# Optimization experiments

Hardware: AMD Instinct MI355X
Metric: run time of the kernel (lower is better)

## Reference

```python
import jax, jax.numpy as jnp
import numpy as np

INV_TEMP = 10.0
_LOG_2PI = float(np.log(2.0 * np.pi))


def log_vmf_norm_const(kappa, dim):
    """log C_dim(kappa) = (dim/2-1)*log(kappa) - (dim/2)*log(2*pi) - log I_{dim/2-1}(kappa),
    with log I_v(kappa) via the uniform asymptotic expansion (as used in mkirchhof/url)."""
    v = dim / 2.0 - 1.0
    s = jnp.sqrt(v * v + kappa * kappa)
    log_iv = s + v * jnp.log(kappa / (v + s)) - 0.5 * _LOG_2PI - 0.25 * jnp.log(v * v + kappa * kappa)
    return v * jnp.log(kappa) - (dim / 2.0) * _LOG_2PI - log_iv


def _normalize(x, eps=1e-12):
    # matches torch F.normalize: x / max(||x||, eps)
    n = jnp.linalg.norm(x, axis=-1, keepdims=True)
    return x / jnp.maximum(n, eps)


def setup_inputs() -> dict:
    key = jax.random.key(0)
    kf, ku, ky, kw, kp = jax.random.split(key, 5)
    B, C, D = 2048, 16384, 128
    features = jax.random.normal(kf, (B, D), jnp.float32)
    unc = jax.random.uniform(ku, (B,), jnp.float32, minval=0.05, maxval=1.0)
    y = jax.random.randint(ky, (B,), 0, C)
    classifier_weight = jax.random.normal(kw, (C, D), jnp.float32)
    pred = jax.random.normal(kp, (B, C), jnp.float32)  # unused by the loss, kept for signature fidelity
    return {"pred": pred, "unc": unc, "y": y, "features": features,
            "classifier_weight": classifier_weight}


def reference(pred, unc, y, features, classifier_weight):
    dim = features.shape[-1]
    class_mu = _normalize(classifier_weight)                                  # [C, D]
    class_kappa = jnp.maximum(jnp.linalg.norm(classifier_weight, axis=-1), 1.0) * INV_TEMP  # [C]
    batch_mu = _normalize(features)                                           # [B, D]
    batch_kappa = 1.0 / unc                                                   # [B]

    # ||k1*mu1 + k2*mu2|| with unit mu's  ==  sqrt(k1^2 + k2^2 + 2*k1*k2*<mu1,mu2>)
    # (avoids the torch code's [B, C, D] broadcast; same math)
    dots = jnp.einsum('bd,cd->bc', batch_mu, class_mu)                        # [B, C]
    k1 = batch_kappa[:, None]                                                 # [B, 1]
    k2 = class_kappa[None, :]                                                 # [1, C]
    kappa3 = jnp.sqrt(jnp.maximum(k1 * k1 + k2 * k2 + 2.0 * k1 * k2 * dots, 1e-12))  # [B, C]

    sim = (log_vmf_norm_const(k1, dim) + log_vmf_norm_const(k2, dim)
           - log_vmf_norm_const(kappa3, dim))                                 # [B, C]

    gathered = jnp.take_along_axis(sim, y[:, None], axis=1)[:, 0]             # [B]
    lse = jax.nn.logsumexp(sim, axis=1)                                       # [B]
    return jnp.mean(-gathered + lse)
```

## Files before the change

kernel.cpp:

```cpp
#include <hip/hip_runtime.h>
#include <hip/hip_bf16.h>


typedef __bf16 bf16;
typedef __attribute__((ext_vector_type(8))) __bf16 bf16x8;
typedef __attribute__((ext_vector_type(4))) float f32x4;
typedef __attribute__((ext_vector_type(2))) float f32x2;

#define LOG2E 1.44269504088896340736f
#define LN2   0.69314718055994530942f
#define VNU   63.0f
#define VSQ   3969.0f

#if __has_builtin(__builtin_amdgcn_exp2f)
#define EXP2F(x) __builtin_amdgcn_exp2f(x)
#else
#define EXP2F(x) exp2f(x)
#endif
#if __has_builtin(__builtin_amdgcn_sqrtf)
#define SQRTF(x) __builtin_amdgcn_sqrtf(x)
#else
#define SQRTF(x) sqrtf(x)
#endif
#if __has_builtin(__builtin_amdgcn_logf)
#define LOG2F(x) __builtin_amdgcn_logf(x)
#else
#define LOG2F(x) __log2f(x)
#endif

#define QC0  289.4379f
#define QC1  -48.9193f
#define QC2  -2.9400f
#define QC3  0.51653f
#define QC4  -0.11373f

__global__ __launch_bounds__(256) void vmf_prep(
    const float* __restrict__ W, const float* __restrict__ feat,
    const float* __restrict__ unc,
    bf16* __restrict__ swW, bf16* __restrict__ swF,
    float4* __restrict__ cst, float* __restrict__ k1, int C, int B)
{
  const int lane = threadIdx.x & 63;
  const int idx  = blockIdx.x * 4 + (threadIdx.x >> 6);
  const bool is_class = idx < C;
  const int b = idx - C;
  const float* src;
  bf16* dstbase;
  int r;
  if (is_class) { src = W + (size_t)idx * 128;  dstbase = swW;  r = idx; }
  else {
    if (b >= B) return;
    src = feat + (size_t)b * 128;  dstbase = swF;  r = b;
  }
  float2 xv = reinterpret_cast<const float2*>(src)[lane];
  float ssq = fmaf(xv.x, xv.x, xv.y * xv.y);
  #pragma unroll
  for (int off = 32; off; off >>= 1) ssq += __shfl_xor(ssq, off);
  float norm = sqrtf(ssq);
  float inv  = 1.0f / fmaxf(norm, 1e-12f);
  __hip_bfloat162 hv = __float22bfloat162_rn(make_float2(xv.x * inv, xv.y * inv));
  {
    const int t   = r >> 4;
    const int l15 = r & 15;
    const int kk  = lane >> 4;
    const int qq  = (lane >> 2) & 3;
    const int j   = 2 * (lane & 3);
    const size_t eoff = (((size_t)(t * 4 + kk)) * 64 + qq * 16 + l15) * 8 + j;
    *reinterpret_cast<__hip_bfloat162*>(dstbase + eoff) = hv;
  }
  if (lane == 0) {
    if (is_class) {
      float kap = fmaxf(norm, 1.0f) * 10.0f;
      float s2  = sqrtf(fmaf(kap, kap, VSQ));
      float f2l = fmaf(VNU, LOG2F(VNU + s2), 0.5f * LOG2F(s2)) - LOG2E * s2;
      cst[idx] = make_float4(2.0f * kap, fmaf(kap, kap, VSQ), f2l, 0.0f);
    } else {
      k1[b] = 1.0f / unc[b];
    }
  }
}

__global__ __launch_bounds__(256, 4) void vmf_main(
    const bf16* __restrict__ swW, const bf16* __restrict__ swF,
    const float4* __restrict__ cst, const float* __restrict__ k1a,
    const int* __restrict__ y, float* __restrict__ partial,
    float* __restrict__ g2, int B, int C, int S)
{
  __shared__ float4 scst[1024];
  const int lane = threadIdx.x & 63;
  const int wave = threadIdx.x >> 6;
  const int q    = lane >> 4;
  const int l15  = lane & 15;

  const int row0 = blockIdx.x * 32 + l15;
  const int row1 = row0 + 16;
  const float k1v0 = k1a[row0], k1v1 = k1a[row1];
  const int yv0 = y[row0], yv1 = y[row1];
  const f32x2 k1pk   = {k1v0, k1v1};
  const f32x2 k1sqpk = k1pk * k1pk;

  const int slice  = blockIdx.y * (C / S);
  for (int i = threadIdx.x; i < 1024; i += 256)
    scst[i] = cst[slice + i];

  bf16x8 bfr[2][4];
  {
    const int rt = blockIdx.x * 2;
    #pragma unroll
    for (int tl = 0; tl < 2; ++tl)
      #pragma unroll
      for (int kk = 0; kk < 4; ++kk)
        bfr[tl][kk] = *reinterpret_cast<const bf16x8*>(
            swF + (((size_t)(rt + tl) * 4 + kk) * 64 + lane) * 8);
  }

  const int nchunk = (C / S) / 64;
  f32x2 sum = {0.f, 0.f};

  int tc = (slice >> 4) + wave;
  bf16x8 af[4];
  #pragma unroll
  for (int kk = 0; kk < 4; ++kk)
    af[kk] = *reinterpret_cast<const bf16x8*>(
        swW + (((size_t)tc * 4 + kk) * 64 + lane) * 8);

  __syncthreads();

  for (int ch = 0; ch < nchunk; ++ch) {
    const int cbase = slice + ch * 64 + wave * 16;
    bf16x8 afn[4];
    if (ch + 1 < nchunk) {
      const int tn = tc + 4;
      #pragma unroll
      for (int kk = 0; kk < 4; ++kk)
        afn[kk] = *reinterpret_cast<const bf16x8*>(
            swW + (((size_t)tn * 4 + kk) * 64 + lane) * 8);
    }
    f32x4 acc0 = {0.f, 0.f, 0.f, 0.f};
    f32x4 acc1 = {0.f, 0.f, 0.f, 0.f};
    #pragma unroll
    for (int kk = 0; kk < 4; ++kk) {
      acc0 = __builtin_amdgcn_mfma_f32_16x16x32_bf16(af[kk], bfr[0][kk], acc0, 0, 0, 0);
      acc1 = __builtin_amdgcn_mfma_f32_16x16x32_bf16(af[kk], bfr[1][kk], acc1, 0, 0, 0);
    }

    f32x2 z[4];
    #pragma unroll
    for (int r = 0; r < 4; ++r) {
      const float4 cv = scst[ch * 64 + wave * 16 + q * 4 + r];
      const f32x2 cvx = {cv.x, cv.x};
      const f32x2 cvy = {cv.y, cv.y};
      const f32x2 cvz = {cv.z, cv.z};
      f32x2 acc2 = {acc0[r], acc1[r]};
      f32x2 u = __builtin_elementwise_fma(cvx * k1pk, acc2, k1sqpk + cvy);
      u = __builtin_elementwise_max(u, (f32x2){VSQ, VSQ});
      f32x2 s3 = {SQRTF(u.x), SQRTF(u.y)};
      f32x2 t  = __builtin_elementwise_fma((f32x2){0.02f, 0.02f}, s3,
                                           (f32x2){-2.7f, -2.7f});
      f32x2 p  = __builtin_elementwise_fma(t, (f32x2){QC4, QC4}, (f32x2){QC3, QC3});
      p = __builtin_elementwise_fma(t, p, (f32x2){QC2, QC2});
      p = __builtin_elementwise_fma(t, p, (f32x2){QC1, QC1});
      p = __builtin_elementwise_fma(t, p, (f32x2){QC0, QC0});
      z[r] = cvz - p;
      sum += (f32x2){EXP2F(z[r].x), EXP2F(z[r].y)};
    }
    if ((yv0 & ~15) == cbase) {
      int rr = (yv0 & 15) - q * 4;
      if (rr >= 0 && rr < 4) {
        float zz = rr == 0 ? z[0].x : rr == 1 ? z[1].x : rr == 2 ? z[2].x : z[3].x;
        g2[row0] = zz;
      }
    }
    if ((yv1 & ~15) == cbase) {
      int rr = (yv1 & 15) - q * 4;
      if (rr >= 0 && rr < 4) {
        float zz = rr == 0 ? z[0].y : rr == 1 ? z[1].y : rr == 2 ? z[2].y : z[3].y;
        g2[row1] = zz;
      }
    }
    #pragma unroll
    for (int kk = 0; kk < 4; ++kk) af[kk] = afn[kk];
    tc += 4;
  }

  float sum0 = sum.x, sum1 = sum.y;
  sum0 += __shfl_xor(sum0, 16); sum0 += __shfl_xor(sum0, 32);
  sum1 += __shfl_xor(sum1, 16); sum1 += __shfl_xor(sum1, 32);

  __shared__ float red[4][32];
  if (lane < 16) { red[wave][l15] = sum0; red[wave][16 + l15] = sum1; }
  __syncthreads();
  if (wave == 0 && lane < 32) {
    float tot = red[0][lane] + red[1][lane] + red[2][lane] + red[3][lane];
    partial[blockIdx.y * B + blockIdx.x * 32 + lane] = tot;
  }
}

__global__ __launch_bounds__(1024) void vmf_finish(
    const float* __restrict__ partial, const float* __restrict__ g2,
    float* __restrict__ out, int B, int S)
{
  float acc = 0.f;
  for (int b = threadIdx.x; b < B; b += 1024) {
    float s = 0.f;
    for (int j = 0; j < S; ++j) s += partial[j * B + b];
    acc += LN2 * (LOG2F(s) - g2[b]);
  }
  #pragma unroll
  for (int off = 32; off; off >>= 1) acc += __shfl_down(acc, off);
  __shared__ float red[16];
  if ((threadIdx.x & 63) == 0) red[threadIdx.x >> 6] = acc;
  __syncthreads();
  if (threadIdx.x < 16) {
    float v = red[threadIdx.x];
    v += __shfl_down(v, 8);
    v += __shfl_down(v, 4);
    v += __shfl_down(v, 2);
    v += __shfl_down(v, 1);
    if (threadIdx.x == 0) out[0] = v / (float)B;
  }
}

extern "C" void kernel_launch(void* const* d_in, const int* in_sizes, int n_in,
                              void* d_out, int out_size, void* d_ws, size_t ws_size,
                              hipStream_t stream)
{
  const float* unc  = (const float*)d_in[1];
  const int*   yin  = (const int*)d_in[2];
  const float* feat = (const float*)d_in[3];
  const float* W    = (const float*)d_in[4];
  const int B = in_sizes[1];
  const int D = 128;
  const int C = in_sizes[4] / D;
  const int S = 16;

  char* ws = (char*)d_ws;
  size_t off = 0;
  auto alloc = [&](size_t bytes) -> void* {
    void* p = ws + off;
    off += (bytes + 255) & ~(size_t)255;
    return p;
  };
  bf16*   swW     = (bf16*)alloc((size_t)C * D * sizeof(bf16));
  bf16*   swF     = (bf16*)alloc((size_t)B * D * sizeof(bf16));
  float4* cstv    = (float4*)alloc((size_t)C * sizeof(float4));
  float*  k1v     = (float*)alloc((size_t)B * 4);
  float*  g2      = (float*)alloc((size_t)B * 4);
  float*  partial = (float*)alloc((size_t)S * B * 4);

  const int prep_blocks = (C + B + 3) / 4;
  vmf_prep<<<prep_blocks, 256, 0, stream>>>(W, feat, unc, swW, swF,
                                            cstv, k1v, C, B);
  dim3 g1(B / 32, S);
  vmf_main<<<g1, 256, 0, stream>>>(swW, swF, cstv, k1v, yin,
                                   partial, g2, B, C, S);
  vmf_finish<<<1, 1024, 0, stream>>>(partial, g2, (float*)d_out, B, S);
}
```

Measured before the change: 204.2 us.

## Fuse classifier normalization into main kernel and swap loop to stationary class tiles

```diff
diff --git a/kernel.cpp b/kernel.cpp
--- a/kernel.cpp
+++ b/kernel.cpp
@@ -34,108 +34,129 @@
 #define QC3  0.51653f
 #define QC4  -0.11373f
 
-__global__ __launch_bounds__(256) void vmf_prep(
-    const float* __restrict__ W, const float* __restrict__ feat,
-    const float* __restrict__ unc,
-    bf16* __restrict__ swW, bf16* __restrict__ swF,
-    float4* __restrict__ cst, float* __restrict__ k1, int C, int B)
+__global__ __launch_bounds__(256) void vmf_prepF(
+    const float* __restrict__ feat, const float* __restrict__ unc,
+    bf16* __restrict__ swF, float* __restrict__ k1,
+    float* __restrict__ sumrow, int B)
 {
   const int lane = threadIdx.x & 63;
-  const int idx  = blockIdx.x * 4 + (threadIdx.x >> 6);
-  const bool is_class = idx < C;
-  const int b = idx - C;
-  const float* src;
-  bf16* dstbase;
-  int r;
-  if (is_class) { src = W + (size_t)idx * 128;  dstbase = swW;  r = idx; }
-  else {
-    if (b >= B) return;
-    src = feat + (size_t)b * 128;  dstbase = swF;  r = b;
-  }
-  float2 xv = reinterpret_cast<const float2*>(src)[lane];
+  const int b    = blockIdx.x * 4 + (threadIdx.x >> 6);
+  if (b >= B) return;
+  float2 xv = reinterpret_cast<const float2*>(feat + (size_t)b * 128)[lane];
   float ssq = fmaf(xv.x, xv.x, xv.y * xv.y);
   #pragma unroll
   for (int off = 32; off; off >>= 1) ssq += __shfl_xor(ssq, off);
-  float norm = sqrtf(ssq);
-  float inv  = 1.0f / fmaxf(norm, 1e-12f);
+  float inv = 1.0f / fmaxf(sqrtf(ssq), 1e-12f);
   __hip_bfloat162 hv = __float22bfloat162_rn(make_float2(xv.x * inv, xv.y * inv));
-  {
-    const int t   = r >> 4;
-    const int l15 = r & 15;
-    const int kk  = lane >> 4;
-    const int qq  = (lane >> 2) & 3;
-    const int j   = 2 * (lane & 3);
-    const size_t eoff = (((size_t)(t * 4 + kk)) * 64 + qq * 16 + l15) * 8 + j;
-    *reinterpret_cast<__hip_bfloat162*>(dstbase + eoff) = hv;
-  }
-  if (lane == 0) {
-    if (is_class) {
-      float kap = fmaxf(norm, 1.0f) * 10.0f;
-      float s2  = sqrtf(fmaf(kap, kap, VSQ));
-      float f2l = fmaf(VNU, LOG2F(VNU + s2), 0.5f * LOG2F(s2)) - LOG2E * s2;
-      cst[idx] = make_float4(2.0f * kap, fmaf(kap, kap, VSQ), f2l, 0.0f);
-    } else {
-      k1[b] = 1.0f / unc[b];
-    }
-  }
+  const int t   = b >> 4;
+  const int l15 = b & 15;
+  const int kk  = lane >> 4;
+  const int qq  = (lane >> 2) & 3;
+  const int j   = 2 * (lane & 3);
+  const size_t eoff = (((size_t)(t * 4 + kk)) * 64 + qq * 16 + l15) * 8 + j;
+  *reinterpret_cast<__hip_bfloat162*>(swF + eoff) = hv;
+  if (lane == 0) k1[b] = 1.0f / unc[b];
+  if (lane == 1) sumrow[b] = 0.0f;
 }
 
 __global__ __launch_bounds__(256, 4) void vmf_main(
-    const bf16* __restrict__ swW, const bf16* __restrict__ swF,
-    const float4* __restrict__ cst, const float* __restrict__ k1a,
-    const int* __restrict__ y, float* __restrict__ partial,
-    float* __restrict__ g2, int B, int C, int S)
-{
-  __shared__ float4 scst[1024];
+    const float* __restrict__ W, const bf16* __restrict__ swF,
+    const float* __restrict__ k1a, const int* __restrict__ y,
+    float* __restrict__ sumrow, float* __restrict__ g2, int B, int NR)
+{
+  __shared__ bf16  ldsA[4][2048];
+  __shared__ float4 ldsC[64];
+  __shared__ float ldsSum[512];
+
   const int lane = threadIdx.x & 63;
   const int wave = threadIdx.x >> 6;
   const int q    = lane >> 4;
   const int l15  = lane & 15;
-
-  const int row0 = blockIdx.x * 32 + l15;
-  const int row1 = row0 + 16;
-  const float k1v0 = k1a[row0], k1v1 = k1a[row1];
-  const int yv0 = y[row0], yv1 = y[row1];
-  const f32x2 k1pk   = {k1v0, k1v1};
-  const f32x2 k1sqpk = k1pk * k1pk;
-
-  const int slice  = blockIdx.y * (C / S);
-  for (int i = threadIdx.x; i < 1024; i += 256)
-    scst[i] = cst[slice + i];
-
+  const int bx   = blockIdx.x;
+
+  {
+    const int r16 = lane >> 2;
+    const int p   = lane & 3;
+    const int gc  = bx * 64 + wave * 16 + r16;
+    const float4* wp = reinterpret_cast<const float4*>(W + (size_t)gc * 128 + p * 32);
+    float4 xv[8];
+    float ssq = 0.f;
+    #pragma unroll
+    for (int i = 0; i < 8; ++i) {
+      xv[i] = wp[i];
+      ssq += xv[i].x * xv[i].x + xv[i].y * xv[i].y +
+             xv[i].z * xv[i].z + xv[i].w * xv[i].w;
+    }
+    ssq += __shfl_xor(ssq, 1);
+    ssq += __shfl_xor(ssq, 2);
+    float norm = sqrtf(ssq);
+    float inv  = 1.0f / fmaxf(norm, 1e-12f);
+    #pragma unroll
+    for (int q2 = 0; q2 < 4; ++q2) {
+      float4 a = xv[2 * q2], c = xv[2 * q2 + 1];
+      __hip_bfloat162 h[4] = {
+        __float22bfloat162_rn(make_float2(a.x * inv, a.y * inv)),
+        __float22bfloat162_rn(make_float2(a.z * inv, a.w * inv)),
+        __float22bfloat162_rn(make_float2(c.x * inv, c.y * inv)),
+        __float22bfloat162_rn(make_float2(c.z * inv, c.w * inv))};
+      *reinterpret_cast<bf16x8*>(&ldsA[wave][(p * 64 + q2 * 16 + r16) * 8]) =
+          *reinterpret_cast<bf16x8*>(h);
+    }
+    if (p == 0) {
+      float kap = fmaxf(norm, 1.0f) * 10.0f;
+      float s2  = sqrtf(fmaf(kap, kap, VSQ));
+      float f2l = fmaf(VNU, LOG2F(VNU + s2), 0.5f * LOG2F(s2)) - LOG2E * s2;
+      ldsC[wave * 16 + r16] = make_float4(2.0f * kap, fmaf(kap, kap, VSQ), f2l, 0.0f);
+    }
+  }
+  for (int i = threadIdx.x; i < NR; i += 256) ldsSum[i] = 0.f;
+  __syncthreads();
+
+  bf16x8 af[4];
+  #pragma unroll
+  for (int kk = 0; kk < 4; ++kk)
+    af[kk] = *reinterpret_cast<bf16x8*>(&ldsA[wave][(kk * 64 + lane) * 8]);
+  f32x2 cvx[4], cvy[4], cvz[4];
+  int cls_lo[4];
+  #pragma unroll
+  for (int r = 0; r < 4; ++r) {
+    float4 c = ldsC[wave * 16 + q * 4 + r];
+    cvx[r] = (f32x2){c.x, c.x};
+    cvy[r] = (f32x2){c.y, c.y};
+    cvz[r] = (f32x2){c.z, c.z};
+    cls_lo[r] = bx * 64 + wave * 16 + q * 4 + r;
+  }
+
+  const int rowbase = blockIdx.y * NR;
+  const int nchunk  = NR / 32;
+  int rt = rowbase >> 4;
   bf16x8 bfr[2][4];
-  {
-    const int rt = blockIdx.x * 2;
-    #pragma unroll
-    for (int tl = 0; tl < 2; ++tl)
+  #pragma unroll
+  for (int tl = 0; tl < 2; ++tl)
+    #pragma unroll
+    for (int kk = 0; kk < 4; ++kk)
+      bfr[tl][kk] = *reinterpret_cast<const bf16x8*>(
+          swF + (((size_t)(rt + tl) * 4 + kk) * 64 + lane) * 8);
+
+  for (int ch = 0; ch < nchunk; ++ch) {
+    const int row0 = rowbase + ch * 32 + l15;
+    const int row1 = row0 + 16;
+    const float k10 = k1a[row0], k11 = k1a[row1];
+    const int   yv0 = y[row0],   yv1 = y[row1];
+    const f32x2 k1pk   = {k10, k11};
+    const f32x2 k1sqpk = k1pk * k1pk;
+
+    bf16x8 bfn[2][4];
+    if (ch + 1 < nchunk) {
+      const int tn = rt + 2;
       #pragma unroll
-      for (int kk = 0; kk < 4; ++kk)
-        bfr[tl][kk] = *reinterpret_cast<const bf16x8*>(
-            swF + (((size_t)(rt + tl) * 4 + kk) * 64 + lane) * 8);
-  }
-
-  const int nchunk = (C / S) / 64;
-  f32x2 sum = {0.f, 0.f};
-
-  int tc = (slice >> 4) + wave;
-  bf16x8 af[4];
-  #pragma unroll
-  for (int kk = 0; kk < 4; ++kk)
-    af[kk] = *reinterpret_cast<const bf16x8*>(
-        swW + (((size_t)tc * 4 + kk) * 64 + lane) * 8);
-
-  __syncthreads();
-
-  for (int ch = 0; ch < nchunk; ++ch) {
-    const int cbase = slice + ch * 64 + wave * 16;
-    bf16x8 afn[4];
-    if (ch + 1 < nchunk) {
-      const int tn = tc + 4;
-      #pragma unroll
-      for (int kk = 0; kk < 4; ++kk)
-        afn[kk] = *reinterpret_cast<const bf16x8*>(
-            swW + (((size_t)tn * 4 + kk) * 64 + lane) * 8);
-    }
+      for (int tl = 0; tl < 2; ++tl)
+        #pragma unroll
+        for (int kk = 0; kk < 4; ++kk)
+          bfn[tl][kk] = *reinterpret_cast<const bf16x8*>(
+              swF + (((size_t)(tn + tl) * 4 + kk) * 64 + lane) * 8);
+    }
+
     f32x4 acc0 = {0.f, 0.f, 0.f, 0.f};
     f32x4 acc1 = {0.f, 0.f, 0.f, 0.f};
     #pragma unroll
@@ -145,14 +166,11 @@
     }
 
     f32x2 z[4];
+    f32x2 sum = {0.f, 0.f};
     #pragma unroll
     for (int r = 0; r < 4; ++r) {
-      const float4 cv = scst[ch * 64 + wave * 16 + q * 4 + r];
-      const f32x2 cvx = {cv.x, cv.x};
-      const f32x2 cvy = {cv.y, cv.y};
-      const f32x2 cvz = {cv.z, cv.z};
       f32x2 acc2 = {acc0[r], acc1[r]};
-      f32x2 u = __builtin_elementwise_fma(cvx * k1pk, acc2, k1sqpk + cvy);
+      f32x2 u = __builtin_elementwise_fma(cvx[r] * k1pk, acc2, k1sqpk + cvy[r]);
       u = __builtin_elementwise_max(u, (f32x2){VSQ, VSQ});
       f32x2 s3 = {SQRTF(u.x), SQRTF(u.y)};
       f32x2 t  = __builtin_elementwise_fma((f32x2){0.02f, 0.02f}, s3,
@@ -161,51 +179,44 @@
       p = __builtin_elementwise_fma(t, p, (f32x2){QC2, QC2});
       p = __builtin_elementwise_fma(t, p, (f32x2){QC1, QC1});
       p = __builtin_elementwise_fma(t, p, (f32x2){QC0, QC0});
-      z[r] = cvz - p;
+      z[r] = cvz[r] - p;
       sum += (f32x2){EXP2F(z[r].x), EXP2F(z[r].y)};
     }
-    if ((yv0 & ~15) == cbase) {
-      int rr = (yv0 & 15) - q * 4;
-      if (rr >= 0 && rr < 4) {
-        float zz = rr == 0 ? z[0].x : rr == 1 ? z[1].x : rr == 2 ? z[2].x : z[3].x;
-        g2[row0] = zz;
-      }
-    }
-    if ((yv1 & ~15) == cbase) {
-      int rr = (yv1 & 15) - q * 4;
-      if (rr >= 0 && rr < 4) {
-        float zz = rr == 0 ? z[0].y : rr == 1 ? z[1].y : rr == 2 ? z[2].y : z[3].y;
-        g2[row1] = zz;
-      }
-    }
-    #pragma unroll
-    for (int kk = 0; kk < 4; ++kk) af[kk] = afn[kk];
-    tc += 4;
-  }
-
-  float sum0 = sum.x, sum1 = sum.y;
-  sum0 += __shfl_xor(sum0, 16); sum0 += __shfl_xor(sum0, 32);
-  sum1 += __shfl_xor(sum1, 16); sum1 += __shfl_xor(sum1, 32);
-
-  __shared__ float red[4][32];
-  if (lane < 16) { red[wave][l15] = sum0; red[wave][16 + l15] = sum1; }
+    if ((yv0 >> 2) == (cls_lo[0] >> 2)) {
+      int rr = yv0 - cls_lo[0];
+      float zz = rr == 0 ? z[0].x : rr == 1 ? z[1].x : rr == 2 ? z[2].x : z[3].x;
+      g2[row0] = zz;
+    }
+    if ((yv1 >> 2) == (cls_lo[0] >> 2)) {
+      int rr = yv1 - cls_lo[0];
+      float zz = rr == 0 ? z[0].y : rr == 1 ? z[1].y : rr == 2 ? z[2].y : z[3].y;
+      g2[row1] = zz;
+    }
+    sum.x += __shfl_xor(sum.x, 16); sum.x += __shfl_xor(sum.x, 32);
+    sum.y += __shfl_xor(sum.y, 16); sum.y += __shfl_xor(sum.y, 32);
+    if (q == 0) {
+      atomicAdd(&ldsSum[ch * 32 + l15], sum.x);
+      atomicAdd(&ldsSum[ch * 32 + 16 + l15], sum.y);
+    }
+    #pragma unroll
+    for (int tl = 0; tl < 2; ++tl)
+      #pragma unroll
+      for (int kk = 0; kk < 4; ++kk) bfr[tl][kk] = bfn[tl][kk];
+    rt += 2;
+  }
+
   __syncthreads();
-  if (wave == 0 && lane < 32) {
-    float tot = red[0][lane] + red[1][lane] + red[2][lane] + red[3][lane];
-    partial[blockIdx.y * B + blockIdx.x * 32 + lane] = tot;
-  }
+  for (int i = threadIdx.x; i < NR; i += 256)
+    atomicAdd(&sumrow[rowbase + i], ldsSum[i]);
 }
 
 __global__ __launch_bounds__(1024) void vmf_finish(
-    const float* __restrict__ partial, const float* __restrict__ g2,
-    float* __restrict__ out, int B, int S)
+    const float* __restrict__ sumrow, const float* __restrict__ g2,
+    float* __restrict__ out, int B)
 {
   float acc = 0.f;
-  for (int b = threadIdx.x; b < B; b += 1024) {
-    float s = 0.f;
-    for (int j = 0; j < S; ++j) s += partial[j * B + b];
-    acc += LN2 * (LOG2F(s) - g2[b]);
-  }
+  for (int b = threadIdx.x; b < B; b += 1024)
+    acc += LN2 * (LOG2F(sumrow[b]) - g2[b]);
   #pragma unroll
   for (int off = 32; off; off >>= 1) acc += __shfl_down(acc, off);
   __shared__ float red[16];
@@ -232,7 +243,8 @@
   const int B = in_sizes[1];
   const int D = 128;
   const int C = in_sizes[4] / D;
-  const int S = 16;
+  const int YS = 4;
+  const int NR = B / YS;
 
   char* ws = (char*)d_ws;
   size_t off = 0;
@@ -241,18 +253,13 @@
     off += (bytes + 255) & ~(size_t)255;
     return p;
   };
-  bf16*   swW     = (bf16*)alloc((size_t)C * D * sizeof(bf16));
-  bf16*   swF     = (bf16*)alloc((size_t)B * D * sizeof(bf16));
-  float4* cstv    = (float4*)alloc((size_t)C * sizeof(float4));
-  float*  k1v     = (float*)alloc((size_t)B * 4);
-  float*  g2      = (float*)alloc((size_t)B * 4);
-  float*  partial = (float*)alloc((size_t)S * B * 4);
-
-  const int prep_blocks = (C + B + 3) / 4;
-  vmf_prep<<<prep_blocks, 256, 0, stream>>>(W, feat, unc, swW, swF,
-                                            cstv, k1v, C, B);
-  dim3 g1(B / 32, S);
-  vmf_main<<<g1, 256, 0, stream>>>(swW, swF, cstv, k1v, yin,
-                                   partial, g2, B, C, S);
-  vmf_finish<<<1, 1024, 0, stream>>>(partial, g2, (float*)d_out, B, S);
-}
+  bf16*  swF    = (bf16*)alloc((size_t)B * D * sizeof(bf16));
+  float* k1v    = (float*)alloc((size_t)B * 4);
+  float* g2     = (float*)alloc((size_t)B * 4);
+  float* sumrow = (float*)alloc((size_t)B * 4);
+
+  vmf_prepF<<<(B + 3) / 4, 256, 0, stream>>>(feat, unc, swF, k1v, sumrow, B);
+  dim3 g1(C / 64, YS);
+  vmf_main<<<g1, 256, 0, stream>>>(W, swF, k1v, yin, sumrow, g2, B, NR);
+  vmf_finish<<<1, 1024, 0, stream>>>(sumrow, g2, (float*)d_out, B);
+}
```

Result: no change. 206.4 us (+1.1%).
